# Optimization experiments

Measured on AMD Instinct MI355X. Metric: run time of the kernel, lower is better.

The kernel has to match this reference:

```python
import jax, jax.numpy as jnp
import numpy as np


def _split_feature(x, ns):
    # channel-last split: [b,h,w,c] -> [b*ns*ns, h/ns, w/ns, c]
    b, h, w, c = x.shape
    hn, wn = h // ns, w // ns
    return x.reshape(b, ns, hn, ns, wn, c).transpose(0, 1, 3, 2, 4, 5).reshape(b * ns * ns, hn, wn, c)


def _merge_splits(x, ns):
    # inverse of _split_feature: [b*ns*ns, h, w, c] -> [b, ns*h, ns*w, c]
    b, h, w, c = x.shape
    nb = b // (ns * ns)
    return x.reshape(nb, ns, ns, h, w, c).transpose(0, 1, 3, 2, 4, 5).reshape(nb, ns * h, ns * w, c)


def _gen_shift_window_attn_mask(h, w, ns):
    # numpy replica of _unimatch_generate_shift_window_attn_mask
    wsh, wsw = h // ns, w // ns
    ssh, ssw = wsh // 2, wsw // 2
    img = np.zeros((1, h, w, 1), dtype=np.float32)
    cnt = 0
    for hs in (slice(0, -wsh), slice(-wsh, -ssh), slice(-ssh, None)):
        for ws in (slice(0, -wsw), slice(-wsw, -ssw), slice(-ssw, None)):
            img[:, hs, ws, :] = cnt
            cnt += 1
    win = img.reshape(1, ns, wsh, ns, wsw, 1).transpose(0, 1, 3, 2, 4, 5).reshape(ns * ns, wsh * wsw)
    am = win[:, None, :] - win[:, :, None]
    return np.where(am != 0, np.float32(-100.0), np.float32(0.0)).astype(np.float32)


def setup_inputs() -> dict:
    key = jax.random.key(0)
    B, H, W, C, NS = 8, 96, 128, 128, 4
    kq, kk, kv = jax.random.split(key, 3)
    q = jax.random.normal(kq, (B, H * W, C), jnp.float32)
    k = jax.random.normal(kk, (B, H * W, C), jnp.float32)
    v = jax.random.normal(kv, (B, H * W, C), jnp.float32)
    attn_mask = jnp.asarray(_gen_shift_window_attn_mask(H, W, NS))  # [NS*NS, n, n]
    return {"q": q, "k": k, "v": v, "attn_mask": attn_mask,
            "num_splits": NS, "with_shift": 1, "h": H, "w": W}


def reference(q, k, v, attn_mask, num_splits, with_shift, h, w):
    b, _, c = q.shape
    ns = num_splits
    wsh, wsw = h // ns, w // ns
    n = wsh * wsw
    bn = b * ns * ns
    q = q.reshape(b, h, w, c)
    k = k.reshape(b, h, w, c)
    v = v.reshape(b, h, w, c)
    if with_shift:
        sh, sw = wsh // 2, wsw // 2
        q = jnp.roll(q, (-sh, -sw), axis=(1, 2))
        k = jnp.roll(k, (-sh, -sw), axis=(1, 2))
        v = jnp.roll(v, (-sh, -sw), axis=(1, 2))
    qf = _split_feature(q, ns).reshape(bn, n, c)
    kf = _split_feature(k, ns).reshape(bn, n, c)
    vf = _split_feature(v, ns).reshape(bn, n, c)
    scale = jnp.asarray(c, qf.dtype) ** 0.5
    scores = jnp.einsum('bnc,bmc->bnm', qf, kf) / scale  # [bn, n, n]
    if with_shift:
        scores = scores + jnp.tile(attn_mask, (b, 1, 1))
    attn = jax.nn.softmax(scores, axis=-1)
    out = jnp.einsum('bnm,bmc->bnc', attn, vf)
    out = _merge_splits(out.reshape(bn, wsh, wsw, c), ns)  # [b, h, w, c]
    if with_shift:
        out = jnp.roll(out, (sh, sw), axis=(1, 2))
    return out.reshape(b, h * w, c)
```

## Files before the change

kernel.cpp:

```cpp
#include <hip/hip_runtime.h>

#define H 96
#define W 128
#define C 128
#define WSH 24
#define WSW 32
#define NTOK 768
#define SH 12
#define SW 16
#define KT 32
#define NKT 24
#define KSTR 160
#define VSTR 40
#define KTILE_B (KT * KSTR * 2)
#define VTILE_B (C * VSTR * 2)
#define UNIT_B  (KTILE_B + VTILE_B)
#define WS_NEED (128L * NKT * UNIT_B)

typedef __attribute__((ext_vector_type(8))) short short8;
typedef __attribute__((ext_vector_type(4))) float floatx4;

__device__ inline unsigned short f2bf(float f) {
  union { float f; unsigned u; } un; un.f = f;
  unsigned r = un.u + 0x7FFF + ((un.u >> 16) & 1);
  return (unsigned short)(r >> 16);
}

__device__ inline int tok_off(int tok, int wh, int ww) {
  int r = tok >> 5;
  int cc = tok & 31;
  int y = wh * WSH + r + SH; if (y >= H) y -= H;
  int x = ww * WSW + cc + SW; if (x >= W) x -= W;
  return y * W + x;
}

__global__ __launch_bounds__(256) void prep_kernel(const float* __restrict__ k,
                                                   const float* __restrict__ v,
                                                   unsigned short* __restrict__ ws) {
  __shared__ unsigned short Vlds[KT][136];
  const int bid = blockIdx.x;
  const int w = bid / NKT;
  const int kt = bid - w * NKT;
  const int batch = w >> 4, win = w & 15;
  const int wh = win >> 2, ww = win & 3;
  int y = wh * WSH + kt + SH; if (y >= H) y -= H;

  const int t = threadIdx.x;
  const int cc = t >> 3;
  const int c0 = (t & 7) * 16;
  int x = ww * WSW + cc + SW; if (x >= W) x -= W;
  const long src = ((long)batch * H * W + (long)y * W + x) * C + c0;
  unsigned short* tile = ws + (long)bid * (UNIT_B / 2);

  {
    const float* kp = k + src;
    short8 o0, o1;
#pragma unroll
    for (int j = 0; j < 2; ++j) {
      floatx4 a = *(const floatx4*)(kp + j * 8);
      floatx4 b = *(const floatx4*)(kp + j * 8 + 4);
      o0[j*4+0] = (short)f2bf(a[0]); o0[j*4+1] = (short)f2bf(a[1]);
      o0[j*4+2] = (short)f2bf(a[2]); o0[j*4+3] = (short)f2bf(a[3]);
      o1[j*4+0] = (short)f2bf(b[0]); o1[j*4+1] = (short)f2bf(b[1]);
      o1[j*4+2] = (short)f2bf(b[2]); o1[j*4+3] = (short)f2bf(b[3]);
    }
    short8 s0, s1;
    s0[0]=o0[0]; s0[1]=o0[1]; s0[2]=o0[2]; s0[3]=o0[3]; s0[4]=o1[0]; s0[5]=o1[1]; s0[6]=o1[2]; s0[7]=o1[3];
    s1[0]=o0[4]; s1[1]=o0[5]; s1[2]=o0[6]; s1[3]=o0[7]; s1[4]=o1[4]; s1[5]=o1[5]; s1[6]=o1[6]; s1[7]=o1[7];
    *(short8*)(tile + cc * KSTR + c0) = s0;
    *(short8*)(tile + cc * KSTR + c0 + 8) = s1;
  }
  {
    const float* vp = v + src;
#pragma unroll
    for (int j = 0; j < 4; ++j) {
      floatx4 a = *(const floatx4*)(vp + j * 4);
      Vlds[cc][c0 + j*4 + 0] = f2bf(a[0]);
      Vlds[cc][c0 + j*4 + 1] = f2bf(a[1]);
      Vlds[cc][c0 + j*4 + 2] = f2bf(a[2]);
      Vlds[cc][c0 + j*4 + 3] = f2bf(a[3]);
    }
  }
  __syncthreads();
  {
    const int c = t >> 1, kh = t & 1;
    unsigned short* vout = tile + (KTILE_B / 2) + c * VSTR + kh * 16;
    short8 o0, o1;
#pragma unroll
    for (int i = 0; i < 8; ++i) o0[i] = (short)Vlds[kh * 16 + i][c];
#pragma unroll
    for (int i = 0; i < 8; ++i) o1[i] = (short)Vlds[kh * 16 + 8 + i][c];
    *(short8*)(vout) = o0;
    *(short8*)(vout + 8) = o1;
  }
}

__global__ __launch_bounds__(256, 3) void attn_main(const float* __restrict__ q,
                                                    const unsigned short* __restrict__ ws,
                                                    float* __restrict__ out) {
  __shared__ unsigned short stage[UNIT_B / 2];
  __shared__ unsigned short Ps[4][2][16 * VSTR];

  const int bid = blockIdx.x;
  const int g = bid / 48;
  const int rm = bid - g * 48;
  const int qt = rm >> 3;
  const int w = g * 8 + (rm & 7);
  const int batch = w >> 4, win = w & 15;
  const int wh = win >> 2, ww = win & 3;

  const int tid = threadIdx.x;
  const int wave = tid >> 6, lane = tid & 63;
  const int col = lane & 15, quad = lane >> 4;
  const long bbase = (long)batch * (H * W * C);

  short8 qfrag[2][4];
#pragma unroll
  for (int s = 0; s < 2; ++s) {
    int qtok = qt * 128 + wave * 32 + s * 16 + col;
    const float* qp = q + bbase + (long)tok_off(qtok, wh, ww) * C + quad * 8;
#pragma unroll
    for (int kc = 0; kc < 4; ++kc) {
      floatx4 a = *(const floatx4*)(qp + kc * 32);
      floatx4 b = *(const floatx4*)(qp + kc * 32 + 4);
      short8 v8;
      v8[0]=(short)f2bf(a[0]); v8[1]=(short)f2bf(a[1]); v8[2]=(short)f2bf(a[2]); v8[3]=(short)f2bf(a[3]);
      v8[4]=(short)f2bf(b[0]); v8[5]=(short)f2bf(b[1]); v8[6]=(short)f2bf(b[2]); v8[7]=(short)f2bf(b[3]);
      qfrag[s][kc] = v8;
    }
  }

  int qreg[2][4];
#pragma unroll
  for (int s = 0; s < 2; ++s)
#pragma unroll
    for (int r = 0; r < 4; ++r) {
      int tok = qt * 128 + wave * 32 + s * 16 + quad * 4 + r;
      int rrq = tok >> 5, ccq = tok & 31;
      int qh = (wh == 3) ? ((rrq >= SH) ? 2 : 1) : 0;
      int qw = (ww == 3) ? ((ccq >= SW) ? 2 : 1) : 0;
      qreg[s][r] = qh * 3 + qw;
    }

  floatx4 oacc[2][8];
#pragma unroll
  for (int s = 0; s < 2; ++s)
#pragma unroll
    for (int i = 0; i < 8; ++i) oacc[s][i] = (floatx4){0.f, 0.f, 0.f, 0.f};
  float lsum[2][4] = {{0.f,0.f,0.f,0.f},{0.f,0.f,0.f,0.f}};

  const unsigned short* wsw_ = ws + (long)(w * NKT) * (UNIT_B / 2);
  auto lds3 = (__attribute__((address_space(3))) char*)&stage[0];
  const unsigned short* Vt = stage + KTILE_B / 2;

  const float SC2 = 0.12751739f;
  const float MNEG = -144.2695041f;

  for (int kt = 0; kt < NKT; ++kt) {
    const unsigned short* gt = wsw_ + (long)kt * (UNIT_B / 2);
    __syncthreads();
#pragma unroll
    for (int j = 0; j < 5; ++j) {
      __builtin_amdgcn_global_load_lds(
          (const __attribute__((address_space(1))) unsigned int*)(gt + (j * 256 + tid) * 8),
          (__attribute__((address_space(3))) unsigned int*)(lds3 + (j * 256 + wave * 64) * 16),
          16, 0, 0);
    }
    __syncthreads();

    floatx4 s00 = (floatx4){0,0,0,0}, s01 = (floatx4){0,0,0,0};
    floatx4 s10 = (floatx4){0,0,0,0}, s11 = (floatx4){0,0,0,0};
#pragma unroll
    for (int kc = 0; kc < 4; ++kc) {
      short8 k0 = *(const short8*)&stage[col * KSTR + kc * 32 + quad * 8];
      short8 k1 = *(const short8*)&stage[(col + 16) * KSTR + kc * 32 + quad * 8];
      s00 = __builtin_amdgcn_mfma_f32_16x16x32_bf16(qfrag[0][kc], k0, s00, 0, 0, 0);
      s01 = __builtin_amdgcn_mfma_f32_16x16x32_bf16(qfrag[0][kc], k1, s01, 0, 0, 0);
      s10 = __builtin_amdgcn_mfma_f32_16x16x32_bf16(qfrag[1][kc], k0, s10, 0, 0, 0);
      s11 = __builtin_amdgcn_mfma_f32_16x16x32_bf16(qfrag[1][kc], k1, s11, 0, 0, 0);
    }

    const int khb = (wh == 3) ? ((kt >= SH) ? 6 : 3) : 0;
    const int kr0 = khb + ((ww == 3) ? 1 : 0);
    const int kr1 = khb + ((ww == 3) ? 2 : 0);

#pragma unroll
    for (int s = 0; s < 2; ++s) {
      const floatx4& a0 = s ? s10 : s00;
      const floatx4& a1 = s ? s11 : s01;
#pragma unroll
      for (int r = 0; r < 4; ++r) {
        float m0 = (qreg[s][r] == kr0) ? 0.f : MNEG;
        float m1 = (qreg[s][r] == kr1) ? 0.f : MNEG;
        float p0 = __builtin_amdgcn_exp2f(fmaf(a0[r], SC2, m0));
        float p1 = __builtin_amdgcn_exp2f(fmaf(a1[r], SC2, m1));
        lsum[s][r] += p0 + p1;
        Ps[wave][s][(quad * 4 + r) * VSTR + col] = f2bf(p0);
        Ps[wave][s][(quad * 4 + r) * VSTR + col + 16] = f2bf(p1);
      }
    }

    short8 pf0 = *(const short8*)&Ps[wave][0][col * VSTR + quad * 8];
    short8 pf1 = *(const short8*)&Ps[wave][1][col * VSTR + quad * 8];
#pragma unroll
    for (int cb = 0; cb < 8; ++cb) {
      short8 vf = *(const short8*)&Vt[(cb * 16 + col) * VSTR + quad * 8];
      oacc[0][cb] = __builtin_amdgcn_mfma_f32_16x16x32_bf16(pf0, vf, oacc[0][cb], 0, 0, 0);
      oacc[1][cb] = __builtin_amdgcn_mfma_f32_16x16x32_bf16(pf1, vf, oacc[1][cb], 0, 0, 0);
    }
  }

#pragma unroll
  for (int s = 0; s < 2; ++s)
#pragma unroll
    for (int r = 0; r < 4; ++r) {
      float l = lsum[s][r];
      l += __shfl_xor(l, 1); l += __shfl_xor(l, 2);
      l += __shfl_xor(l, 4); l += __shfl_xor(l, 8);
      float inv = 1.0f / l;
      int tok = qt * 128 + wave * 32 + s * 16 + quad * 4 + r;
      float* op = out + bbase + (long)tok_off(tok, wh, ww) * C + col;
#pragma unroll
      for (int cb = 0; cb < 8; ++cb) op[cb * 16] = oacc[s][cb][r] * inv;
    }
}

#define KSTRF 136
#define VSTRF 40
#define PSTRF 40
__global__ __launch_bounds__(256, 2) void attn_fallback(
    const float* __restrict__ q, const float* __restrict__ k,
    const float* __restrict__ v, const float* __restrict__ mask,
    float* __restrict__ out) {
  __shared__ unsigned short Ks[KT * KSTRF];
  __shared__ unsigned short Vtl[C * VSTRF];
  __shared__ unsigned short Psf[4][16 * PSTRF];
  const int qtile = blockIdx.x;
  const int beta  = blockIdx.y;
  const int batch = beta >> 4;
  const int win   = beta & 15;
  const int wh = win >> 2, ww = win & 3;
  const int tid = threadIdx.x;
  const int wave = tid >> 6, lane = tid & 63;
  const int col = lane & 15, quad = lane >> 4;
  const long bbase = (long)batch * (H * W * C);
  const int qtok = qtile * 64 + wave * 16 + col;
  const float* qp = q + bbase + (long)tok_off(qtok, wh, ww) * C + quad * 8;
  short8 qfrag[4];
#pragma unroll
  for (int kc = 0; kc < 4; ++kc) {
    floatx4 a = *(const floatx4*)(qp + kc * 32);
    floatx4 b = *(const floatx4*)(qp + kc * 32 + 4);
    short8 s;
    s[0]=f2bf(a[0]); s[1]=f2bf(a[1]); s[2]=f2bf(a[2]); s[3]=f2bf(a[3]);
    s[4]=f2bf(b[0]); s[5]=f2bf(b[1]); s[6]=f2bf(b[2]); s[7]=f2bf(b[3]);
    qfrag[kc] = s;
  }
  floatx4 oacc[8];
#pragma unroll
  for (int i = 0; i < 8; ++i) oacc[i] = (floatx4){0.f,0.f,0.f,0.f};
  float mrow[4], lrow[4];
#pragma unroll
  for (int r = 0; r < 4; ++r) { mrow[r] = -1e30f; lrow[r] = 0.f; }
  const int skey = tid >> 3;
  const int sch  = (tid & 7) * 4;
  const float invscale = 0.088388347648318447f;
  const float* maskw = mask + (long)win * (NTOK * NTOK);
  const int qrow_m = qtile * 64 + wave * 16 + quad * 4;
  for (int kt = 0; kt < NKT; ++kt) {
    const int ktok0 = kt * KT;
    const long srow = bbase + (long)tok_off(ktok0 + skey, wh, ww) * C;
    const float* kp = k + srow;
    const float* vp = v + srow;
    __syncthreads();
#pragma unroll
    for (int j = 0; j < 4; ++j) {
      floatx4 f = *(const floatx4*)(kp + sch + j * 32);
      unsigned lo = (unsigned)f2bf(f[0]) | ((unsigned)f2bf(f[1]) << 16);
      unsigned hi = (unsigned)f2bf(f[2]) | ((unsigned)f2bf(f[3]) << 16);
      *(uint2*)&Ks[skey * KSTRF + sch + j * 32] = make_uint2(lo, hi);
    }
#pragma unroll
    for (int j = 0; j < 4; ++j) {
      floatx4 f = *(const floatx4*)(vp + sch + j * 32);
      int chb = sch + j * 32;
      Vtl[(chb + 0) * VSTRF + skey] = f2bf(f[0]);
      Vtl[(chb + 1) * VSTRF + skey] = f2bf(f[1]);
      Vtl[(chb + 2) * VSTRF + skey] = f2bf(f[2]);
      Vtl[(chb + 3) * VSTRF + skey] = f2bf(f[3]);
    }
    __syncthreads();
    floatx4 s0 = (floatx4){0.f,0.f,0.f,0.f};
    floatx4 s1 = (floatx4){0.f,0.f,0.f,0.f};
#pragma unroll
    for (int kc = 0; kc < 4; ++kc) {
      short8 k0 = *(const short8*)&Ks[col * KSTRF + kc * 32 + quad * 8];
      short8 k1 = *(const short8*)&Ks[(col + 16) * KSTRF + kc * 32 + quad * 8];
      s0 = __builtin_amdgcn_mfma_f32_16x16x32_bf16(qfrag[kc], k0, s0, 0, 0, 0);
      s1 = __builtin_amdgcn_mfma_f32_16x16x32_bf16(qfrag[kc], k1, s1, 0, 0, 0);
    }
    float mk0[4], mk1[4];
    const float* mp = maskw + (long)qrow_m * NTOK + ktok0 + col;
#pragma unroll
    for (int r = 0; r < 4; ++r) { mk0[r] = mp[r * NTOK]; mk1[r] = mp[r * NTOK + 16]; }
#pragma unroll
    for (int r = 0; r < 4; ++r) {
      float a0 = s0[r] * invscale + mk0[r];
      float a1 = s1[r] * invscale + mk1[r];
      float mx = fmaxf(a0, a1);
      mx = fmaxf(mx, __shfl_xor(mx, 1)); mx = fmaxf(mx, __shfl_xor(mx, 2));
      mx = fmaxf(mx, __shfl_xor(mx, 4)); mx = fmaxf(mx, __shfl_xor(mx, 8));
      float mnew = fmaxf(mrow[r], mx);
      float alpha = __expf(mrow[r] - mnew);
      float p0 = __expf(a0 - mnew);
      float p1 = __expf(a1 - mnew);
      float rs = p0 + p1;
      rs += __shfl_xor(rs, 1); rs += __shfl_xor(rs, 2);
      rs += __shfl_xor(rs, 4); rs += __shfl_xor(rs, 8);
      lrow[r] = lrow[r] * alpha + rs;
      mrow[r] = mnew;
#pragma unroll
      for (int cb = 0; cb < 8; ++cb) oacc[cb][r] *= alpha;
      Psf[wave][(quad * 4 + r) * PSTRF + col]      = f2bf(p0);
      Psf[wave][(quad * 4 + r) * PSTRF + 16 + col] = f2bf(p1);
    }
    __syncthreads();
    short8 pf = *(const short8*)&Psf[wave][col * PSTRF + quad * 8];
#pragma unroll
    for (int cb = 0; cb < 8; ++cb) {
      short8 vf = *(const short8*)&Vtl[(cb * 16 + col) * VSTRF + quad * 8];
      oacc[cb] = __builtin_amdgcn_mfma_f32_16x16x32_bf16(pf, vf, oacc[cb], 0, 0, 0);
    }
  }
#pragma unroll
  for (int r = 0; r < 4; ++r) {
    float inv_l = 1.0f / lrow[r];
    int tok = qtile * 64 + wave * 16 + quad * 4 + r;
    float* op = out + bbase + (long)tok_off(tok, wh, ww) * C + col;
#pragma unroll
    for (int cb = 0; cb < 8; ++cb) op[cb * 16] = oacc[cb][r] * inv_l;
  }
}

extern "C" void kernel_launch(void* const* d_in, const int* in_sizes, int n_in,
                              void* d_out, int out_size, void* d_ws, size_t ws_size,
                              hipStream_t stream) {
  const float* q    = (const float*)d_in[0];
  const float* k    = (const float*)d_in[1];
  const float* v    = (const float*)d_in[2];
  const float* mask = (const float*)d_in[3];
  float* out = (float*)d_out;
  if (ws_size >= (size_t)WS_NEED) {
    prep_kernel<<<128 * NKT, 256, 0, stream>>>(k, v, (unsigned short*)d_ws);
    attn_main<<<768, 256, 0, stream>>>(q, (const unsigned short*)d_ws, out);
  } else {
    attn_fallback<<<dim3(12, 128), dim3(256), 0, stream>>>(q, k, v, mask, out);
  }
}
```

Measured before the change: 267.0 us.

## Double-buffer K/V LDS staging and precompute per-phase shift masks

Adds a second LDS stage buffer so the async global-to-LDS load of the next K/V tile is issued while the current tile is computed, leaving one barrier per iteration instead of two. The V transpose in the prep kernel interleaves key rows so P can be written to LDS as packed 32-bit pairs, halving the LDS stores. Mask offsets are precomputed into registers per query row for the two key-row phases, so the per-tile comparisons go away. The cost is more LDS per block, which may lower occupancy, and extra mask registers.

```diff
diff --git a/kernel.cpp b/kernel.cpp
--- a/kernel.cpp
+++ b/kernel.cpp
@@ -87,9 +87,9 @@
     unsigned short* vout = tile + (KTILE_B / 2) + c * VSTR + kh * 16;
     short8 o0, o1;
 #pragma unroll
-    for (int i = 0; i < 8; ++i) o0[i] = (short)Vlds[kh * 16 + i][c];
-#pragma unroll
-    for (int i = 0; i < 8; ++i) o1[i] = (short)Vlds[kh * 16 + 8 + i][c];
+    for (int i = 0; i < 8; ++i) o0[i] = (short)Vlds[(i & 1) * 16 + kh * 8 + (i >> 1)][c];
+#pragma unroll
+    for (int i = 0; i < 8; ++i) o1[i] = (short)Vlds[(i & 1) * 16 + kh * 8 + 4 + (i >> 1)][c];
     *(short8*)(vout) = o0;
     *(short8*)(vout + 8) = o1;
   }
@@ -98,7 +98,7 @@
 __global__ __launch_bounds__(256, 3) void attn_main(const float* __restrict__ q,
                                                     const unsigned short* __restrict__ ws,
                                                     float* __restrict__ out) {
-  __shared__ unsigned short stage[UNIT_B / 2];
+  __shared__ unsigned short stage[2][UNIT_B / 2];
   __shared__ unsigned short Ps[4][2][16 * VSTR];
 
   const int bid = blockIdx.x;
@@ -130,7 +130,10 @@
     }
   }
 
-  int qreg[2][4];
+  const float MNEG = -144.2695041f;
+  const float SC2 = 0.12751739f;
+
+  float mPh[2][2][8];
 #pragma unroll
   for (int s = 0; s < 2; ++s)
 #pragma unroll
@@ -139,7 +142,13 @@
       int rrq = tok >> 5, ccq = tok & 31;
       int qh = (wh == 3) ? ((rrq >= SH) ? 2 : 1) : 0;
       int qw = (ww == 3) ? ((ccq >= SW) ? 2 : 1) : 0;
-      qreg[s][r] = qh * 3 + qw;
+      int qreg = qh * 3 + qw;
+      int c0b = (ww == 3) ? 1 : 0, c1b = (ww == 3) ? 2 : 0;
+      int hA = (wh == 3) ? 3 : 0, hB = (wh == 3) ? 6 : 0;
+      mPh[0][0][s * 4 + r] = (qreg == hA + c0b) ? 0.f : MNEG;
+      mPh[0][1][s * 4 + r] = (qreg == hA + c1b) ? 0.f : MNEG;
+      mPh[1][0][s * 4 + r] = (qreg == hB + c0b) ? 0.f : MNEG;
+      mPh[1][1][s * 4 + r] = (qreg == hB + c1b) ? 0.f : MNEG;
     }
 
   floatx4 oacc[2][8];
@@ -150,15 +159,10 @@
   float lsum[2][4] = {{0.f,0.f,0.f,0.f},{0.f,0.f,0.f,0.f}};
 
   const unsigned short* wsw_ = ws + (long)(w * NKT) * (UNIT_B / 2);
-  auto lds3 = (__attribute__((address_space(3))) char*)&stage[0];
-  const unsigned short* Vt = stage + KTILE_B / 2;
-
-  const float SC2 = 0.12751739f;
-  const float MNEG = -144.2695041f;
-
-  for (int kt = 0; kt < NKT; ++kt) {
+
+  auto stage_issue = [&](int kt, int buf) {
     const unsigned short* gt = wsw_ + (long)kt * (UNIT_B / 2);
-    __syncthreads();
+    auto lds3 = (__attribute__((address_space(3))) char*)&stage[buf][0];
 #pragma unroll
     for (int j = 0; j < 5; ++j) {
       __builtin_amdgcn_global_load_lds(
@@ -166,37 +170,39 @@
           (__attribute__((address_space(3))) unsigned int*)(lds3 + (j * 256 + wave * 64) * 16),
           16, 0, 0);
     }
+  };
+
+  auto tile_step = [&](int kt, const float (&m01)[2][8]) {
+    const int cur = kt & 1;
     __syncthreads();
+    if (kt + 1 < NKT) stage_issue(kt + 1, cur ^ 1);
+
+    const unsigned short* Kt = &stage[cur][0];
+    const unsigned short* Vt = &stage[cur][KTILE_B / 2];
 
     floatx4 s00 = (floatx4){0,0,0,0}, s01 = (floatx4){0,0,0,0};
     floatx4 s10 = (floatx4){0,0,0,0}, s11 = (floatx4){0,0,0,0};
 #pragma unroll
     for (int kc = 0; kc < 4; ++kc) {
-      short8 k0 = *(const short8*)&stage[col * KSTR + kc * 32 + quad * 8];
-      short8 k1 = *(const short8*)&stage[(col + 16) * KSTR + kc * 32 + quad * 8];
+      short8 k0 = *(const short8*)&Kt[col * KSTR + kc * 32 + quad * 8];
+      short8 k1 = *(const short8*)&Kt[(col + 16) * KSTR + kc * 32 + quad * 8];
       s00 = __builtin_amdgcn_mfma_f32_16x16x32_bf16(qfrag[0][kc], k0, s00, 0, 0, 0);
       s01 = __builtin_amdgcn_mfma_f32_16x16x32_bf16(qfrag[0][kc], k1, s01, 0, 0, 0);
       s10 = __builtin_amdgcn_mfma_f32_16x16x32_bf16(qfrag[1][kc], k0, s10, 0, 0, 0);
       s11 = __builtin_amdgcn_mfma_f32_16x16x32_bf16(qfrag[1][kc], k1, s11, 0, 0, 0);
     }
 
-    const int khb = (wh == 3) ? ((kt >= SH) ? 6 : 3) : 0;
-    const int kr0 = khb + ((ww == 3) ? 1 : 0);
-    const int kr1 = khb + ((ww == 3) ? 2 : 0);
-
 #pragma unroll
     for (int s = 0; s < 2; ++s) {
       const floatx4& a0 = s ? s10 : s00;
       const floatx4& a1 = s ? s11 : s01;
 #pragma unroll
       for (int r = 0; r < 4; ++r) {
-        float m0 = (qreg[s][r] == kr0) ? 0.f : MNEG;
-        float m1 = (qreg[s][r] == kr1) ? 0.f : MNEG;
-        float p0 = __builtin_amdgcn_exp2f(fmaf(a0[r], SC2, m0));
-        float p1 = __builtin_amdgcn_exp2f(fmaf(a1[r], SC2, m1));
+        float p0 = __builtin_amdgcn_exp2f(fmaf(a0[r], SC2, m01[0][s * 4 + r]));
+        float p1 = __builtin_amdgcn_exp2f(fmaf(a1[r], SC2, m01[1][s * 4 + r]));
         lsum[s][r] += p0 + p1;
-        Ps[wave][s][(quad * 4 + r) * VSTR + col] = f2bf(p0);
-        Ps[wave][s][(quad * 4 + r) * VSTR + col + 16] = f2bf(p1);
+        unsigned pk = (unsigned)f2bf(p0) | ((unsigned)f2bf(p1) << 16);
+        *(unsigned*)&Ps[wave][s][(quad * 4 + r) * VSTR + 2 * col] = pk;
       }
     }
 
@@ -208,7 +214,11 @@
       oacc[0][cb] = __builtin_amdgcn_mfma_f32_16x16x32_bf16(pf0, vf, oacc[0][cb], 0, 0, 0);
       oacc[1][cb] = __builtin_amdgcn_mfma_f32_16x16x32_bf16(pf1, vf, oacc[1][cb], 0, 0, 0);
     }
-  }
+  };
+
+  stage_issue(0, 0);
+  for (int kt = 0; kt < SH; ++kt)  tile_step(kt, mPh[0]);
+  for (int kt = SH; kt < NKT; ++kt) tile_step(kt, mPh[1]);
 
 #pragma unroll
   for (int s = 0; s < 2; ++s)
```

After: 262.0 us. Within noise of the previous version (-1.9%).

## Load pre-swizzled K/V fragments directly from global into registers, larger per-wave query tiles

Applied to the files above, without the earlier changes.

The prep kernel now writes K and V tiles in MFMA-fragment order, so the attention kernel loads them straight from global memory into registers and no longer stages them through LDS with barriers. Each wave now handles 96 query rows (6 sub-tiles) instead of 32, and blocks shrink to 128 threads with 512 blocks. The next key tile is prefetched into registers during the PV step. This removes the per-tile __syncthreads and LDS staging and amortizes each K/V load over more queries. In exchange, register pressure rises sharply (48 accumulator vectors plus 24 Q fragments), occupancy drops, and there are fewer blocks to spread across CUs.

```diff
diff --git a/kernel.cpp b/kernel.cpp
--- a/kernel.cpp
+++ b/kernel.cpp
@@ -10,12 +10,9 @@
 #define SW 16
 #define KT 32
 #define NKT 24
-#define KSTR 160
-#define VSTR 40
-#define KTILE_B (KT * KSTR * 2)
-#define VTILE_B (C * VSTR * 2)
-#define UNIT_B  (KTILE_B + VTILE_B)
-#define WS_NEED (128L * NKT * UNIT_B)
+#define PSTR 40
+#define TILE_USH 8192
+#define WS_NEED (128L * NKT * TILE_USH * 2)
 
 typedef __attribute__((ext_vector_type(8))) short short8;
 typedef __attribute__((ext_vector_type(4))) float floatx4;
@@ -46,66 +43,73 @@
   int y = wh * WSH + kt + SH; if (y >= H) y -= H;
 
   const int t = threadIdx.x;
-  const int cc = t >> 3;
-  const int c0 = (t & 7) * 16;
-  int x = ww * WSW + cc + SW; if (x >= W) x -= W;
+  const int key = t >> 3;
+  const int j = t & 7;
+  const int c0 = j * 16;
+  int x = ww * WSW + key + SW; if (x >= W) x -= W;
   const long src = ((long)batch * H * W + (long)y * W + x) * C + c0;
-  unsigned short* tile = ws + (long)bid * (UNIT_B / 2);
+  unsigned short* tile = ws + (long)bid * TILE_USH;
 
   {
     const float* kp = k + src;
+    short8 s0, s1;
+#pragma unroll
+    for (int i = 0; i < 2; ++i) {
+      floatx4 a = *(const floatx4*)(kp + i * 8);
+      floatx4 b = *(const floatx4*)(kp + i * 8 + 4);
+      s0[i*4+0] = (short)f2bf(a[0]); s0[i*4+1] = (short)f2bf(a[1]);
+      s0[i*4+2] = (short)f2bf(a[2]); s0[i*4+3] = (short)f2bf(a[3]);
+      s1[i*4+0] = (short)f2bf(b[0]); s1[i*4+1] = (short)f2bf(b[1]);
+      s1[i*4+2] = (short)f2bf(b[2]); s1[i*4+3] = (short)f2bf(b[3]);
+    }
     short8 o0, o1;
-#pragma unroll
-    for (int j = 0; j < 2; ++j) {
-      floatx4 a = *(const floatx4*)(kp + j * 8);
-      floatx4 b = *(const floatx4*)(kp + j * 8 + 4);
-      o0[j*4+0] = (short)f2bf(a[0]); o0[j*4+1] = (short)f2bf(a[1]);
-      o0[j*4+2] = (short)f2bf(a[2]); o0[j*4+3] = (short)f2bf(a[3]);
-      o1[j*4+0] = (short)f2bf(b[0]); o1[j*4+1] = (short)f2bf(b[1]);
-      o1[j*4+2] = (short)f2bf(b[2]); o1[j*4+3] = (short)f2bf(b[3]);
-    }
-    short8 s0, s1;
-    s0[0]=o0[0]; s0[1]=o0[1]; s0[2]=o0[2]; s0[3]=o0[3]; s0[4]=o1[0]; s0[5]=o1[1]; s0[6]=o1[2]; s0[7]=o1[3];
-    s1[0]=o0[4]; s1[1]=o0[5]; s1[2]=o0[6]; s1[3]=o0[7]; s1[4]=o1[4]; s1[5]=o1[5]; s1[6]=o1[6]; s1[7]=o1[7];
-    *(short8*)(tile + cc * KSTR + c0) = s0;
-    *(short8*)(tile + cc * KSTR + c0 + 8) = s1;
+    o0[0]=s0[0]; o0[1]=s0[1]; o0[2]=s0[2]; o0[3]=s0[3]; o0[4]=s1[0]; o0[5]=s1[1]; o0[6]=s1[2]; o0[7]=s1[3];
+    o1[0]=s0[4]; o1[1]=s0[5]; o1[2]=s0[6]; o1[3]=s0[7]; o1[4]=s1[4]; o1[5]=s1[5]; o1[6]=s1[6]; o1[7]=s1[7];
+    const int kc = j >> 1;
+    const int q2 = (j & 1) * 2;
+    unsigned short* kout = tile + kc * 1024 + key * 32 + q2 * 8;
+    *(short8*)(kout) = o0;
+    *(short8*)(kout + 8) = o1;
   }
   {
     const float* vp = v + src;
 #pragma unroll
-    for (int j = 0; j < 4; ++j) {
-      floatx4 a = *(const floatx4*)(vp + j * 4);
-      Vlds[cc][c0 + j*4 + 0] = f2bf(a[0]);
-      Vlds[cc][c0 + j*4 + 1] = f2bf(a[1]);
-      Vlds[cc][c0 + j*4 + 2] = f2bf(a[2]);
-      Vlds[cc][c0 + j*4 + 3] = f2bf(a[3]);
+    for (int i = 0; i < 4; ++i) {
+      floatx4 a = *(const floatx4*)(vp + i * 4);
+      Vlds[key][c0 + i*4 + 0] = f2bf(a[0]);
+      Vlds[key][c0 + i*4 + 1] = f2bf(a[1]);
+      Vlds[key][c0 + i*4 + 2] = f2bf(a[2]);
+      Vlds[key][c0 + i*4 + 3] = f2bf(a[3]);
     }
   }
   __syncthreads();
   {
-    const int c = t >> 1, kh = t & 1;
-    unsigned short* vout = tile + (KTILE_B / 2) + c * VSTR + kh * 16;
-    short8 o0, o1;
-#pragma unroll
-    for (int i = 0; i < 8; ++i) o0[i] = (short)Vlds[kh * 16 + i][c];
-#pragma unroll
-    for (int i = 0; i < 8; ++i) o1[i] = (short)Vlds[kh * 16 + 8 + i][c];
-    *(short8*)(vout) = o0;
-    *(short8*)(vout + 8) = o1;
-  }
-}
-
-__global__ __launch_bounds__(256, 3) void attn_main(const float* __restrict__ q,
+    const int cb = t >> 5;
+    const int rem = t & 31;
+    const int col = rem >> 1, qh = rem & 1;
+    const int ch = cb * 16 + col;
+#pragma unroll
+    for (int qs = 0; qs < 2; ++qs) {
+      const int quad = qh * 2 + qs;
+      short8 o;
+#pragma unroll
+      for (int i = 0; i < 8; ++i)
+        o[i] = (short)Vlds[(i & 1) * 16 + quad * 4 + (i >> 1)][ch];
+      *(short8*)(tile + 4096 + cb * 512 + (col * 4 + quad) * 8) = o;
+    }
+  }
+}
+
+__global__ __launch_bounds__(128, 1) void attn_main(const float* __restrict__ q,
                                                     const unsigned short* __restrict__ ws,
                                                     float* __restrict__ out) {
-  __shared__ unsigned short stage[UNIT_B / 2];
-  __shared__ unsigned short Ps[4][2][16 * VSTR];
+  __shared__ unsigned short Ps[2][6][16 * PSTR];
 
   const int bid = blockIdx.x;
-  const int g = bid / 48;
-  const int rm = bid - g * 48;
-  const int qt = rm >> 3;
-  const int w = g * 8 + (rm & 7);
+  const int x8 = bid & 7;
+  const int i = bid >> 3;
+  const int w = x8 * 16 + (i & 15);
+  const int qb = i >> 4;
   const int batch = w >> 4, win = w & 15;
   const int wh = win >> 2, ww = win & 3;
 
@@ -113,11 +117,13 @@
   const int wave = tid >> 6, lane = tid & 63;
   const int col = lane & 15, quad = lane >> 4;
   const long bbase = (long)batch * (H * W * C);
-
-  short8 qfrag[2][4];
-#pragma unroll
-  for (int s = 0; s < 2; ++s) {
-    int qtok = qt * 128 + wave * 32 + s * 16 + col;
+  const int qbase = qb * 192 + wave * 96;
+  const int loff = (col * 4 + quad) * 8;
+
+  short8 qfrag[6][4];
+#pragma unroll
+  for (int s = 0; s < 6; ++s) {
+    const int qtok = qbase + s * 16 + col;
     const float* qp = q + bbase + (long)tok_off(qtok, wh, ww) * C + quad * 8;
 #pragma unroll
     for (int kc = 0; kc < 4; ++kc) {
@@ -130,95 +136,92 @@
     }
   }
 
-  int qreg[2][4];
-#pragma unroll
-  for (int s = 0; s < 2; ++s)
-#pragma unroll
-    for (int r = 0; r < 4; ++r) {
-      int tok = qt * 128 + wave * 32 + s * 16 + quad * 4 + r;
-      int rrq = tok >> 5, ccq = tok & 31;
-      int qh = (wh == 3) ? ((rrq >= SH) ? 2 : 1) : 0;
-      int qw = (ww == 3) ? ((ccq >= SW) ? 2 : 1) : 0;
-      qreg[s][r] = qh * 3 + qw;
-    }
-
-  floatx4 oacc[2][8];
-#pragma unroll
-  for (int s = 0; s < 2; ++s)
-#pragma unroll
-    for (int i = 0; i < 8; ++i) oacc[s][i] = (floatx4){0.f, 0.f, 0.f, 0.f};
-  float lsum[2][4] = {{0.f,0.f,0.f,0.f},{0.f,0.f,0.f,0.f}};
-
-  const unsigned short* wsw_ = ws + (long)(w * NKT) * (UNIT_B / 2);
-  auto lds3 = (__attribute__((address_space(3))) char*)&stage[0];
-  const unsigned short* Vt = stage + KTILE_B / 2;
-
+  int qreg[6];
+#pragma unroll
+  for (int s = 0; s < 6; ++s) {
+    int rr_s = (qbase >> 5) + (s >> 1);
+    int qh = (wh == 3) ? ((rr_s >= SH) ? 2 : 1) : 0;
+    int qw = (ww == 3) ? ((s & 1) ? 2 : 1) : 0;
+    qreg[s] = qh * 3 + qw;
+  }
+  const int cw0 = (ww == 3) ? 1 : 0, cw1 = (ww == 3) ? 2 : 0;
+  const float MNEG = -144.2695041f;
   const float SC2 = 0.12751739f;
-  const float MNEG = -144.2695041f;
+
+  floatx4 oacc[6][8];
+#pragma unroll
+  for (int s = 0; s < 6; ++s)
+#pragma unroll
+    for (int cb = 0; cb < 8; ++cb) oacc[s][cb] = (floatx4){0.f, 0.f, 0.f, 0.f};
+  float lsum[6][4];
+#pragma unroll
+  for (int s = 0; s < 6; ++s)
+#pragma unroll
+    for (int r = 0; r < 4; ++r) lsum[s][r] = 0.f;
+
+  const unsigned short* wsw_ = ws + (long)w * (NKT * TILE_USH);
+
+  short8 kf0[4], kf1[4];
+  auto load_k = [&](int kt) {
+    const unsigned short* tk = wsw_ + ((long)kt << 13);
+#pragma unroll
+    for (int kc = 0; kc < 4; ++kc) {
+      kf0[kc] = *(const short8*)(tk + kc * 1024 + loff);
+      kf1[kc] = *(const short8*)(tk + kc * 1024 + 512 + loff);
+    }
+  };
+  load_k(0);
 
   for (int kt = 0; kt < NKT; ++kt) {
-    const unsigned short* gt = wsw_ + (long)kt * (UNIT_B / 2);
-    __syncthreads();
-#pragma unroll
-    for (int j = 0; j < 5; ++j) {
-      __builtin_amdgcn_global_load_lds(
-          (const __attribute__((address_space(1))) unsigned int*)(gt + (j * 256 + tid) * 8),
-          (__attribute__((address_space(3))) unsigned int*)(lds3 + (j * 256 + wave * 64) * 16),
-          16, 0, 0);
-    }
-    __syncthreads();
-
-    floatx4 s00 = (floatx4){0,0,0,0}, s01 = (floatx4){0,0,0,0};
-    floatx4 s10 = (floatx4){0,0,0,0}, s11 = (floatx4){0,0,0,0};
-#pragma unroll
-    for (int kc = 0; kc < 4; ++kc) {
-      short8 k0 = *(const short8*)&stage[col * KSTR + kc * 32 + quad * 8];
-      short8 k1 = *(const short8*)&stage[(col + 16) * KSTR + kc * 32 + quad * 8];
-      s00 = __builtin_amdgcn_mfma_f32_16x16x32_bf16(qfrag[0][kc], k0, s00, 0, 0, 0);
-      s01 = __builtin_amdgcn_mfma_f32_16x16x32_bf16(qfrag[0][kc], k1, s01, 0, 0, 0);
-      s10 = __builtin_amdgcn_mfma_f32_16x16x32_bf16(qfrag[1][kc], k0, s10, 0, 0, 0);
-      s11 = __builtin_amdgcn_mfma_f32_16x16x32_bf16(qfrag[1][kc], k1, s11, 0, 0, 0);
-    }
+    const unsigned short* tv = wsw_ + ((long)kt << 13) + 4096;
+    short8 vf[8];
+#pragma unroll
+    for (int cb = 0; cb < 8; ++cb) vf[cb] = *(const short8*)(tv + cb * 512 + loff);
 
     const int khb = (wh == 3) ? ((kt >= SH) ? 6 : 3) : 0;
-    const int kr0 = khb + ((ww == 3) ? 1 : 0);
-    const int kr1 = khb + ((ww == 3) ? 2 : 0);
-
-#pragma unroll
-    for (int s = 0; s < 2; ++s) {
-      const floatx4& a0 = s ? s10 : s00;
-      const floatx4& a1 = s ? s11 : s01;
+    const int kr0 = khb + cw0, kr1 = khb + cw1;
+
+#pragma unroll
+    for (int s = 0; s < 6; ++s) {
+      floatx4 a0 = (floatx4){0.f, 0.f, 0.f, 0.f};
+      floatx4 a1 = (floatx4){0.f, 0.f, 0.f, 0.f};
+#pragma unroll
+      for (int kc = 0; kc < 4; ++kc) {
+        a0 = __builtin_amdgcn_mfma_f32_16x16x32_bf16(qfrag[s][kc], kf0[kc], a0, 0, 0, 0);
+        a1 = __builtin_amdgcn_mfma_f32_16x16x32_bf16(qfrag[s][kc], kf1[kc], a1, 0, 0, 0);
+      }
+      const float m0 = (qreg[s] == kr0) ? 0.f : MNEG;
+      const float m1 = (qreg[s] == kr1) ? 0.f : MNEG;
 #pragma unroll
       for (int r = 0; r < 4; ++r) {
-        float m0 = (qreg[s][r] == kr0) ? 0.f : MNEG;
-        float m1 = (qreg[s][r] == kr1) ? 0.f : MNEG;
         float p0 = __builtin_amdgcn_exp2f(fmaf(a0[r], SC2, m0));
         float p1 = __builtin_amdgcn_exp2f(fmaf(a1[r], SC2, m1));
         lsum[s][r] += p0 + p1;
-        Ps[wave][s][(quad * 4 + r) * VSTR + col] = f2bf(p0);
-        Ps[wave][s][(quad * 4 + r) * VSTR + col + 16] = f2bf(p1);
+        unsigned pk = (unsigned)f2bf(p0) | ((unsigned)f2bf(p1) << 16);
+        *(unsigned*)&Ps[wave][s][(quad * 4 + r) * PSTR + 2 * col] = pk;
       }
     }
 
-    short8 pf0 = *(const short8*)&Ps[wave][0][col * VSTR + quad * 8];
-    short8 pf1 = *(const short8*)&Ps[wave][1][col * VSTR + quad * 8];
-#pragma unroll
-    for (int cb = 0; cb < 8; ++cb) {
-      short8 vf = *(const short8*)&Vt[(cb * 16 + col) * VSTR + quad * 8];
-      oacc[0][cb] = __builtin_amdgcn_mfma_f32_16x16x32_bf16(pf0, vf, oacc[0][cb], 0, 0, 0);
-      oacc[1][cb] = __builtin_amdgcn_mfma_f32_16x16x32_bf16(pf1, vf, oacc[1][cb], 0, 0, 0);
-    }
-  }
-
-#pragma unroll
-  for (int s = 0; s < 2; ++s)
+    if (kt + 1 < NKT) load_k(kt + 1);
+
+#pragma unroll
+    for (int s = 0; s < 6; ++s) {
+      short8 pf = *(const short8*)&Ps[wave][s][col * PSTR + quad * 8];
+#pragma unroll
+      for (int cb = 0; cb < 8; ++cb)
+        oacc[s][cb] = __builtin_amdgcn_mfma_f32_16x16x32_bf16(pf, vf[cb], oacc[s][cb], 0, 0, 0);
+    }
+  }
+
+#pragma unroll
+  for (int s = 0; s < 6; ++s)
 #pragma unroll
     for (int r = 0; r < 4; ++r) {
       float l = lsum[s][r];
       l += __shfl_xor(l, 1); l += __shfl_xor(l, 2);
       l += __shfl_xor(l, 4); l += __shfl_xor(l, 8);
       float inv = 1.0f / l;
-      int tok = qt * 128 + wave * 32 + s * 16 + quad * 4 + r;
+      int tok = qbase + s * 16 + quad * 4 + r;
       float* op = out + bbase + (long)tok_off(tok, wh, ww) * C + col;
 #pragma unroll
       for (int cb = 0; cb < 8; ++cb) op[cb * 16] = oacc[s][cb][r] * inv;
@@ -352,7 +355,7 @@
   float* out = (float*)d_out;
   if (ws_size >= (size_t)WS_NEED) {
     prep_kernel<<<128 * NKT, 256, 0, stream>>>(k, v, (unsigned short*)d_ws);
-    attn_main<<<768, 256, 0, stream>>>(q, (const unsigned short*)d_ws, out);
+    attn_main<<<512, 128, 0, stream>>>(q, (const unsigned short*)d_ws, out);
   } else {
     attn_fallback<<<dim3(12, 128), dim3(256), 0, stream>>>(q, k, v, mask, out);
   }
```

New measurement: 248.2 us. 7.1% less time.
